# Kernel optimization log

Measured on AMD Instinct MI355X. Metric: run time of the kernel, lower is better.

## Reference

```python
import jax, jax.numpy as jnp
import numpy as np

N_NODES = 50000
IN_CH = 256
N_REL = 5
N_EDGES = 800000
LAST_SENSES = 25000
LAST_GLOBALS = 45000


def setup_inputs() -> dict:
    key = jax.random.key(0)
    ks = jax.random.split(key, 12)
    batch_x = jax.random.normal(ks[0], (N_NODES, IN_CH), dtype=jnp.float32)
    batch_edge_index = jax.random.randint(ks[1], (2, N_EDGES), 0, N_NODES)
    batch_edge_type = jax.random.randint(ks[2], (N_EDGES,), 0, N_REL)
    s = 1.0 / np.sqrt(IN_CH)
    comp = jax.random.normal(ks[3], (N_REL, N_REL), dtype=jnp.float32) * (1.0 / np.sqrt(N_REL))
    basis = jax.random.normal(ks[4], (N_REL, IN_CH, IN_CH), dtype=jnp.float32) * s
    root = jax.random.normal(ks[5], (IN_CH, IN_CH), dtype=jnp.float32) * s
    bias = jnp.zeros((IN_CH,), dtype=jnp.float32)
    n_glob = LAST_GLOBALS - LAST_SENSES
    Wg = jax.random.normal(ks[6], (n_glob, IN_CH), dtype=jnp.float32) * s
    bg = jnp.zeros((n_glob,), dtype=jnp.float32)
    Ws = jax.random.normal(ks[7], (LAST_SENSES, IN_CH), dtype=jnp.float32) * s
    bs = jnp.zeros((LAST_SENSES,), dtype=jnp.float32)
    return {
        'batch_x': batch_x,
        'batch_edge_index': batch_edge_index,
        'batch_edge_type': batch_edge_type,
        'comp': comp,
        'basis': basis,
        'root': root,
        'bias': bias,
        'Wg': Wg,
        'bg': bg,
        'Ws': Ws,
        'bs': bs,
    }


def _rgcn_conv(x, edge_index, edge_type, comp, basis, root, bias):
    # Basis decomposition: W_r = sum_b comp[r,b] * basis[b]  -> [R, d, d]
    R = comp.shape[0]
    N = x.shape[0]
    W = jnp.einsum('rb,bdf->rdf', comp, basis)
    # Transform all nodes by every relation weight once ([R,N,F]), then gather
    # per edge instead of doing an [E,d,d] weight gather.
    H = jnp.einsum('nd,rdf->rnf', x, W)
    src, dst = edge_index[0], edge_index[1]
    msgs = H[edge_type, src]                     # [E, F]
    seg = edge_type * N + dst                    # combined (relation, dst) id
    sums = jax.ops.segment_sum(msgs, seg, num_segments=R * N)
    cnt = jax.ops.segment_sum(jnp.ones((msgs.shape[0],), msgs.dtype), seg,
                              num_segments=R * N)
    mean = sums / jnp.maximum(cnt, 1.0)[:, None]  # per-relation mean aggregation
    agg = mean.reshape(R, N, -1).sum(axis=0)
    return agg + x @ root + bias


def reference(batch_x, batch_edge_index, batch_edge_type, comp, basis, root,
              bias, Wg, bg, Ws, bs):
    h = jax.nn.relu(_rgcn_conv(batch_x, batch_edge_index, batch_edge_type,
                               comp, basis, root, bias))
    x1 = h[0]                                    # current node embedding [F]
    logits_global = Wg @ x1 + bg
    logits_sense = Ws @ x1 + bs
    return (jax.nn.log_softmax(logits_global, axis=0),
            jax.nn.log_softmax(logits_sense, axis=0))
```

## Files before the change

kernel.cpp:

```cpp
#include <hip/hip_runtime.h>
#include <math.h>

#define N_NODES 50000
#define IN_CH 256
#define N_REL 5
#define N_EDGES 800000
#define N_GLOB 20000
#define N_SENSE 25000
#define N_OUT 45000
#define MAX_MATCH 256
#define LOGIT_BLOCKS 2048
#define NWAVES (LOGIT_BLOCKS * 4)
#define N_OUT4 (N_OUT / 4)
#define N_GLOB4 (N_GLOB / 4)


__device__ __forceinline__ void record_edge(const int* ei, const int* et,
                                            int* ip, int e) {
    int t = et[e];
    int p = atomicAdd(&ip[0], 1);
    if (p < MAX_MATCH) {
        ip[8 + p] = ei[e];
        ip[8 + MAX_MATCH + p] = t;
    }
    atomicAdd(&ip[1 + t], 1);
}

__global__ void k_scan(const int* __restrict__ ei,
                       const int* __restrict__ et,
                       int* __restrict__ ip) {
    int e4 = blockIdx.x * 256 + threadIdx.x;
    if (e4 * 4 >= N_EDGES) return;
    int4 d = ((const int4*)(ei + N_EDGES))[e4];
    int e = e4 * 4;
    if (d.x == 0) record_edge(ei, et, ip, e);
    if (d.y == 0) record_edge(ei, et, ip, e + 1);
    if (d.z == 0) record_edge(ei, et, ip, e + 2);
    if (d.w == 0) record_edge(ei, et, ip, e + 3);
}

__global__ void k_x1(const float* __restrict__ x,
                     const float* __restrict__ comp,
                     const float* __restrict__ basis,
                     const float* __restrict__ root,
                     const float* __restrict__ bias,
                     const int* __restrict__ ip,
                     float* __restrict__ x1acc) {
    __shared__ float u[64];
    int tid = threadIdx.x;
    int mat = blockIdx.x >> 2;
    int d0 = (blockIdx.x & 3) * 64;
    if (tid < 64) {
        if (mat < 5) {
            int m = ip[0]; if (m > MAX_MATCH) m = MAX_MATCH;
            float acc = 0.f;
            for (int j = 0; j < m; ++j) {
                int s = ip[8 + j];
                int t = ip[8 + MAX_MATCH + j];
                float scale = comp[t * N_REL + mat] /
                              fmaxf((float)ip[1 + t], 1.0f);
                acc += scale * x[(size_t)s * IN_CH + d0 + tid];
            }
            u[tid] = acc;
        } else {
            u[tid] = x[d0 + tid];
        }
    }
    __syncthreads();
    const float* M = ((mat < 5) ? (basis + (size_t)mat * IN_CH * IN_CH)
                                : root) + (size_t)d0 * IN_CH;
    float acc = 0.f;
#pragma unroll 16
    for (int d = 0; d < 64; ++d) acc += u[d] * M[d * IN_CH + tid];
    if (mat == 5 && d0 == 0) acc += bias[tid];
    atomicAdd(&x1acc[tid], acc);
}

__global__ void k_logits(const float* __restrict__ Wg,
                         const float* __restrict__ bg,
                         const float* __restrict__ Ws,
                         const float* __restrict__ bs,
                         const float* __restrict__ x1acc,
                         float* __restrict__ raw) {
    int tid = threadIdx.x, lane = tid & 63;
    int gw = blockIdx.x * 4 + (tid >> 6);
    float4 xv = ((const float4*)x1acc)[lane];
    xv.x = fmaxf(xv.x, 0.f); xv.y = fmaxf(xv.y, 0.f);
    xv.z = fmaxf(xv.z, 0.f); xv.w = fmaxf(xv.w, 0.f);
    for (int row = gw; row < N_OUT; row += NWAVES) {
        const float4* wr;
        float b;
        if (row < N_GLOB) {
            wr = (const float4*)(Wg + (size_t)row * IN_CH);
            b = bg[row];
        } else {
            int r2 = row - N_GLOB;
            wr = (const float4*)(Ws + (size_t)r2 * IN_CH);
            b = bs[r2];
        }
        float4 wv = wr[lane];
        float s = wv.x * xv.x + wv.y * xv.y + wv.z * xv.z + wv.w * xv.w;
#pragma unroll
        for (int off = 32; off > 0; off >>= 1) s += __shfl_down(s, off);
        if (lane == 0) raw[row] = s + b;
    }
}

__global__ void k_statsfinal(const float* __restrict__ raw,
                             float* __restrict__ out) {
    __shared__ float r1[256], r2[256];
    int tid = threadIdx.x;
    const float4* o4 = (const float4*)raw;
    float mg = -3.4e38f, ms = -3.4e38f;
    for (int i = tid; i < N_OUT4; i += 256) {
        float4 v = o4[i];
        float m4 = fmaxf(fmaxf(v.x, v.y), fmaxf(v.z, v.w));
        if (i < N_GLOB4) mg = fmaxf(mg, m4); else ms = fmaxf(ms, m4);
    }
    r1[tid] = mg; r2[tid] = ms; __syncthreads();
    for (int h = 128; h > 0; h >>= 1) {
        if (tid < h) {
            r1[tid] = fmaxf(r1[tid], r1[tid + h]);
            r2[tid] = fmaxf(r2[tid], r2[tid + h]);
        }
        __syncthreads();
    }
    mg = r1[0]; ms = r2[0]; __syncthreads();
    float sg = 0.f, ss = 0.f;
    for (int i = tid; i < N_OUT4; i += 256) {
        float4 v = o4[i];
        if (i < N_GLOB4)
            sg += expf(v.x - mg) + expf(v.y - mg) + expf(v.z - mg) + expf(v.w - mg);
        else
            ss += expf(v.x - ms) + expf(v.y - ms) + expf(v.z - ms) + expf(v.w - ms);
    }
    r1[tid] = sg; r2[tid] = ss; __syncthreads();
    for (int h = 128; h > 0; h >>= 1) {
        if (tid < h) { r1[tid] += r1[tid + h]; r2[tid] += r2[tid + h]; }
        __syncthreads();
    }
    float zg = mg + logf(r1[0]);
    float zs = ms + logf(r2[0]);
    int i = blockIdx.x * 256 + tid;
    if (i < N_OUT4) {
        float4 v = o4[i];
        float z = (i < N_GLOB4) ? zg : zs;
        v.x -= z; v.y -= z; v.z -= z; v.w -= z;
        ((float4*)out)[i] = v;
    }
}

extern "C" void kernel_launch(void* const* d_in, const int* in_sizes, int n_in,
                              void* d_out, int out_size, void* d_ws, size_t ws_size,
                              hipStream_t stream) {
    const float* x     = (const float*)d_in[0];
    const int*   ei    = (const int*)  d_in[1];
    const int*   et    = (const int*)  d_in[2];
    const float* comp  = (const float*)d_in[3];
    const float* basis = (const float*)d_in[4];
    const float* root  = (const float*)d_in[5];
    const float* bias  = (const float*)d_in[6];
    const float* Wg    = (const float*)d_in[7];
    const float* bg    = (const float*)d_in[8];
    const float* Wsn   = (const float*)d_in[9];
    const float* bs    = (const float*)d_in[10];
    float* out = (float*)d_out;

    float* base  = (float*)d_ws;
    float* x1acc = base;
    int*   ip    = (int*)(base + 256);
    float* raw   = base + 1024;

    hipMemsetAsync(d_ws, 0, 1056, stream);
    k_scan      <<<(N_EDGES / 4 + 255) / 256, 256, 0, stream>>>(ei, et, ip);
    k_x1        <<<24, 256, 0, stream>>>(x, comp, basis, root, bias, ip, x1acc);
    k_logits    <<<LOGIT_BLOCKS, 256, 0, stream>>>(Wg, bg, Wsn, bs, x1acc, raw);
    k_statsfinal<<<(N_OUT4 + 255) / 256, 256, 0, stream>>>(raw, out);
}
```

Before: 170.8 us.

## Fuse scan, x1, logits and log-softmax into one cooperative kernel

Replaces the memset and four separate kernel launches with a single cooperative kernel on a fixed grid of 1024 blocks. The stages are separated by grid-wide syncs, and block 0 zeroes the workspace in-kernel instead of a separate memset. The scan also skips the per-element checks when none of the four destinations in an int4 is node 0. The aim is to remove per-launch overhead and inter-kernel gaps, at the cost of four grid barriers and a fixed grid size that must stay fully co-resident.

```diff
diff --git a/kernel.cpp b/kernel.cpp
--- a/kernel.cpp
+++ b/kernel.cpp
@@ -1,5 +1,8 @@
 #include <hip/hip_runtime.h>
+#include <hip/hip_cooperative_groups.h>
 #include <math.h>
+
+namespace cg = cooperative_groups;
 
 #define N_NODES 50000
 #define IN_CH 256
@@ -9,144 +12,163 @@
 #define N_SENSE 25000
 #define N_OUT 45000
 #define MAX_MATCH 256
-#define LOGIT_BLOCKS 2048
-#define NWAVES (LOGIT_BLOCKS * 4)
+#define GRID_BLOCKS 1024
+#define NWAVES (GRID_BLOCKS * 4)
 #define N_OUT4 (N_OUT / 4)
 #define N_GLOB4 (N_GLOB / 4)
-
-
-__device__ __forceinline__ void record_edge(const int* ei, const int* et,
-                                            int* ip, int e) {
-    int t = et[e];
-    int p = atomicAdd(&ip[0], 1);
-    if (p < MAX_MATCH) {
-        ip[8 + p] = ei[e];
-        ip[8 + MAX_MATCH + p] = t;
-    }
-    atomicAdd(&ip[1 + t], 1);
-}
-
-__global__ void k_scan(const int* __restrict__ ei,
-                       const int* __restrict__ et,
-                       int* __restrict__ ip) {
-    int e4 = blockIdx.x * 256 + threadIdx.x;
-    if (e4 * 4 >= N_EDGES) return;
-    int4 d = ((const int4*)(ei + N_EDGES))[e4];
-    int e = e4 * 4;
-    if (d.x == 0) record_edge(ei, et, ip, e);
-    if (d.y == 0) record_edge(ei, et, ip, e + 1);
-    if (d.z == 0) record_edge(ei, et, ip, e + 2);
-    if (d.w == 0) record_edge(ei, et, ip, e + 3);
-}
-
-__global__ void k_x1(const float* __restrict__ x,
-                     const float* __restrict__ comp,
-                     const float* __restrict__ basis,
-                     const float* __restrict__ root,
-                     const float* __restrict__ bias,
-                     const int* __restrict__ ip,
-                     float* __restrict__ x1acc) {
+#define STAT_BLOCKS ((N_OUT4 + 255) / 256)
+
+
+__global__ __launch_bounds__(256, 4)
+void k_fused(const float* __restrict__ x,
+             const int* __restrict__ ei,
+             const int* __restrict__ et,
+             const float* __restrict__ comp,
+             const float* __restrict__ basis,
+             const float* __restrict__ root,
+             const float* __restrict__ bias,
+             const float* __restrict__ Wg,
+             const float* __restrict__ bg,
+             const float* __restrict__ Ws,
+             const float* __restrict__ bs,
+             float* __restrict__ out,
+             float* __restrict__ x1acc,
+             int* __restrict__ ip,
+             float* __restrict__ raw) {
+    cg::grid_group grid = cg::this_grid();
     __shared__ float u[64];
-    int tid = threadIdx.x;
-    int mat = blockIdx.x >> 2;
-    int d0 = (blockIdx.x & 3) * 64;
-    if (tid < 64) {
-        if (mat < 5) {
-            int m = ip[0]; if (m > MAX_MATCH) m = MAX_MATCH;
-            float acc = 0.f;
-            for (int j = 0; j < m; ++j) {
-                int s = ip[8 + j];
-                int t = ip[8 + MAX_MATCH + j];
-                float scale = comp[t * N_REL + mat] /
-                              fmaxf((float)ip[1 + t], 1.0f);
-                acc += scale * x[(size_t)s * IN_CH + d0 + tid];
-            }
-            u[tid] = acc;
-        } else {
-            u[tid] = x[d0 + tid];
-        }
-    }
-    __syncthreads();
-    const float* M = ((mat < 5) ? (basis + (size_t)mat * IN_CH * IN_CH)
-                                : root) + (size_t)d0 * IN_CH;
-    float acc = 0.f;
+    __shared__ float r1[256], r2[256];
+    int tid = threadIdx.x, bid = blockIdx.x;
+
+    if (bid == 0) {
+        x1acc[tid] = 0.f;
+        if (tid < 8) ip[tid] = 0;
+    }
+    grid.sync();
+
+    {
+        int g = bid * 256 + tid;
+        if (g < N_EDGES / 4) {
+            int4 d = ((const int4*)(ei + N_EDGES))[g];
+            int e = g * 4;
+            int hit4 = (d.x == 0) | (d.y == 0) | (d.z == 0) | (d.w == 0);
+            if (hit4) {
+                #pragma unroll
+                for (int q = 0; q < 4; ++q) {
+                    int dv = (q == 0) ? d.x : (q == 1) ? d.y : (q == 2) ? d.z : d.w;
+                    if (dv == 0) {
+                        int t = et[e + q];
+                        int p = atomicAdd(&ip[0], 1);
+                        if (p < MAX_MATCH) {
+                            ip[8 + p] = ei[e + q];
+                            ip[8 + MAX_MATCH + p] = t;
+                        }
+                        atomicAdd(&ip[1 + t], 1);
+                    }
+                }
+            }
+        }
+    }
+    grid.sync();
+
+    if (bid < 24) {
+        int mat = bid >> 2;
+        int d0 = (bid & 3) * 64;
+        if (tid < 64) {
+            if (mat < 5) {
+                int m = ip[0]; if (m > MAX_MATCH) m = MAX_MATCH;
+                float acc = 0.f;
+                for (int j = 0; j < m; ++j) {
+                    int s = ip[8 + j];
+                    int t = ip[8 + MAX_MATCH + j];
+                    float scale = comp[t * N_REL + mat] /
+                                  fmaxf((float)ip[1 + t], 1.0f);
+                    acc += scale * x[(size_t)s * IN_CH + d0 + tid];
+                }
+                u[tid] = acc;
+            } else {
+                u[tid] = x[d0 + tid];
+            }
+        }
+        __syncthreads();
+        const float* M = ((mat < 5) ? (basis + (size_t)mat * IN_CH * IN_CH)
+                                    : root) + (size_t)d0 * IN_CH;
+        float acc = 0.f;
 #pragma unroll 16
-    for (int d = 0; d < 64; ++d) acc += u[d] * M[d * IN_CH + tid];
-    if (mat == 5 && d0 == 0) acc += bias[tid];
-    atomicAdd(&x1acc[tid], acc);
-}
-
-__global__ void k_logits(const float* __restrict__ Wg,
-                         const float* __restrict__ bg,
-                         const float* __restrict__ Ws,
-                         const float* __restrict__ bs,
-                         const float* __restrict__ x1acc,
-                         float* __restrict__ raw) {
-    int tid = threadIdx.x, lane = tid & 63;
-    int gw = blockIdx.x * 4 + (tid >> 6);
-    float4 xv = ((const float4*)x1acc)[lane];
-    xv.x = fmaxf(xv.x, 0.f); xv.y = fmaxf(xv.y, 0.f);
-    xv.z = fmaxf(xv.z, 0.f); xv.w = fmaxf(xv.w, 0.f);
-    for (int row = gw; row < N_OUT; row += NWAVES) {
-        const float4* wr;
-        float b;
-        if (row < N_GLOB) {
-            wr = (const float4*)(Wg + (size_t)row * IN_CH);
-            b = bg[row];
-        } else {
-            int r2 = row - N_GLOB;
-            wr = (const float4*)(Ws + (size_t)r2 * IN_CH);
-            b = bs[r2];
-        }
-        float4 wv = wr[lane];
-        float s = wv.x * xv.x + wv.y * xv.y + wv.z * xv.z + wv.w * xv.w;
+        for (int d = 0; d < 64; ++d) acc += u[d] * M[d * IN_CH + tid];
+        if (mat == 5 && d0 == 0) acc += bias[tid];
+        atomicAdd(&x1acc[tid], acc);
+    }
+    grid.sync();
+
+    {
+        int lane = tid & 63;
+        int gw = bid * 4 + (tid >> 6);
+        float4 xv = ((const float4*)x1acc)[lane];
+        xv.x = fmaxf(xv.x, 0.f); xv.y = fmaxf(xv.y, 0.f);
+        xv.z = fmaxf(xv.z, 0.f); xv.w = fmaxf(xv.w, 0.f);
+        for (int row = gw; row < N_OUT; row += NWAVES) {
+            const float4* wr;
+            float b;
+            if (row < N_GLOB) {
+                wr = (const float4*)(Wg + (size_t)row * IN_CH);
+                b = bg[row];
+            } else {
+                int r2i = row - N_GLOB;
+                wr = (const float4*)(Ws + (size_t)r2i * IN_CH);
+                b = bs[r2i];
+            }
+            float4 wv = wr[lane];
+            float s = wv.x * xv.x + wv.y * xv.y + wv.z * xv.z + wv.w * xv.w;
 #pragma unroll
-        for (int off = 32; off > 0; off >>= 1) s += __shfl_down(s, off);
-        if (lane == 0) raw[row] = s + b;
-    }
-}
-
-__global__ void k_statsfinal(const float* __restrict__ raw,
-                             float* __restrict__ out) {
-    __shared__ float r1[256], r2[256];
-    int tid = threadIdx.x;
-    const float4* o4 = (const float4*)raw;
-    float mg = -3.4e38f, ms = -3.4e38f;
-    for (int i = tid; i < N_OUT4; i += 256) {
-        float4 v = o4[i];
-        float m4 = fmaxf(fmaxf(v.x, v.y), fmaxf(v.z, v.w));
-        if (i < N_GLOB4) mg = fmaxf(mg, m4); else ms = fmaxf(ms, m4);
-    }
-    r1[tid] = mg; r2[tid] = ms; __syncthreads();
-    for (int h = 128; h > 0; h >>= 1) {
-        if (tid < h) {
-            r1[tid] = fmaxf(r1[tid], r1[tid + h]);
-            r2[tid] = fmaxf(r2[tid], r2[tid + h]);
-        }
-        __syncthreads();
-    }
-    mg = r1[0]; ms = r2[0]; __syncthreads();
-    float sg = 0.f, ss = 0.f;
-    for (int i = tid; i < N_OUT4; i += 256) {
-        float4 v = o4[i];
-        if (i < N_GLOB4)
-            sg += expf(v.x - mg) + expf(v.y - mg) + expf(v.z - mg) + expf(v.w - mg);
-        else
-            ss += expf(v.x - ms) + expf(v.y - ms) + expf(v.z - ms) + expf(v.w - ms);
-    }
-    r1[tid] = sg; r2[tid] = ss; __syncthreads();
-    for (int h = 128; h > 0; h >>= 1) {
-        if (tid < h) { r1[tid] += r1[tid + h]; r2[tid] += r2[tid + h]; }
-        __syncthreads();
-    }
-    float zg = mg + logf(r1[0]);
-    float zs = ms + logf(r2[0]);
-    int i = blockIdx.x * 256 + tid;
-    if (i < N_OUT4) {
-        float4 v = o4[i];
-        float z = (i < N_GLOB4) ? zg : zs;
-        v.x -= z; v.y -= z; v.z -= z; v.w -= z;
-        ((float4*)out)[i] = v;
+            for (int off = 32; off > 0; off >>= 1) s += __shfl_down(s, off);
+            if (lane == 0) raw[row] = s + b;
+        }
+    }
+    grid.sync();
+
+    if (bid >= STAT_BLOCKS) return;
+    {
+        const float4* o4 = (const float4*)raw;
+        float mg = -3.4e38f, ms = -3.4e38f;
+        for (int i = tid; i < N_OUT4; i += 256) {
+            float4 v = o4[i];
+            float m4 = fmaxf(fmaxf(v.x, v.y), fmaxf(v.z, v.w));
+            if (i < N_GLOB4) mg = fmaxf(mg, m4); else ms = fmaxf(ms, m4);
+        }
+        r1[tid] = mg; r2[tid] = ms; __syncthreads();
+        for (int h = 128; h > 0; h >>= 1) {
+            if (tid < h) {
+                r1[tid] = fmaxf(r1[tid], r1[tid + h]);
+                r2[tid] = fmaxf(r2[tid], r2[tid + h]);
+            }
+            __syncthreads();
+        }
+        mg = r1[0]; ms = r2[0]; __syncthreads();
+        float sg = 0.f, ss = 0.f;
+        for (int i = tid; i < N_OUT4; i += 256) {
+            float4 v = o4[i];
+            if (i < N_GLOB4)
+                sg += expf(v.x - mg) + expf(v.y - mg) +
+                      expf(v.z - mg) + expf(v.w - mg);
+            else
+                ss += expf(v.x - ms) + expf(v.y - ms) +
+                      expf(v.z - ms) + expf(v.w - ms);
+        }
+        r1[tid] = sg; r2[tid] = ss; __syncthreads();
+        for (int h = 128; h > 0; h >>= 1) {
+            if (tid < h) { r1[tid] += r1[tid + h]; r2[tid] += r2[tid + h]; }
+            __syncthreads();
+        }
+        float zg = mg + logf(r1[0]);
+        float zs = ms + logf(r2[0]);
+        int i = bid * 256 + tid;
+        if (i < N_OUT4) {
+            float4 v = o4[i];
+            float z = (i < N_GLOB4) ? zg : zs;
+            v.x -= z; v.y -= z; v.z -= z; v.w -= z;
+            ((float4*)out)[i] = v;
+        }
     }
 }
 
@@ -171,9 +193,11 @@
     int*   ip    = (int*)(base + 256);
     float* raw   = base + 1024;
 
-    hipMemsetAsync(d_ws, 0, 1056, stream);
-    k_scan      <<<(N_EDGES / 4 + 255) / 256, 256, 0, stream>>>(ei, et, ip);
-    k_x1        <<<24, 256, 0, stream>>>(x, comp, basis, root, bias, ip, x1acc);
-    k_logits    <<<LOGIT_BLOCKS, 256, 0, stream>>>(Wg, bg, Wsn, bs, x1acc, raw);
-    k_statsfinal<<<(N_OUT4 + 255) / 256, 256, 0, stream>>>(raw, out);
+    void* args[] = {
+        (void*)&x, (void*)&ei, (void*)&et, (void*)&comp, (void*)&basis,
+        (void*)&root, (void*)&bias, (void*)&Wg, (void*)&bg, (void*)&Wsn,
+        (void*)&bs, (void*)&out, (void*)&x1acc, (void*)&ip, (void*)&raw
+    };
+    hipLaunchCooperativeKernel((const void*)k_fused, dim3(GRID_BLOCKS),
+                               dim3(256), args, 0, stream);
 }
```

Result: slower. 550.4 us (+222.2%).
